# Kernel optimization log

Hardware: AMD Instinct MI355X
Metric: run time of the kernel (lower is better)

Reference implementation:

```python
import jax, jax.numpy as jnp
import numpy as np

N, E, F, B = 4096, 8192, 256, 16


def setup_inputs() -> dict:
    key = jax.random.key(0)
    k_x, k_idx, k_w, k_b = jax.random.split(key, 4)
    x = jax.random.normal(k_x, (B, E, F), dtype=jnp.float32)
    # Incidence matrix: each edge (column) connects 2 random distinct nodes.
    ends = jax.random.randint(k_idx, (2, E), 0, N)  # [2, E] node ids per edge
    cols = jnp.arange(E)
    inci = jnp.zeros((N, E), dtype=jnp.float32)
    inci = inci.at[ends[0], cols].set(1.0).at[ends[1], cols].set(1.0)
    w = jax.random.normal(k_w, (N, E), dtype=jnp.float32) * 0.05
    b = jax.random.normal(k_b, (N, E), dtype=jnp.float32) * 0.01
    return {"x": x, "inci": inci, "w": w, "b": b}


def reference(x, inci, w, b):
    # (w * inci + b) @ x : [N,E] x [B,E,F] -> [B,N,F]
    m = w * inci + b
    return jnp.einsum("ne,bef->bnf", m, x)
```

## Files before the change

kernel.cpp:

```cpp
#include <hip/hip_runtime.h>
#include <hip/hip_bf16.h>

#define Ndim 4096
#define Edim 8192
#define Fdim 256
#define Bdim 16
#define EB (Edim * 2)
#define NT (Edim / 64)

typedef __attribute__((ext_vector_type(8))) short bf16x8;
typedef __attribute__((ext_vector_type(4))) float f32x4;

__device__ __forceinline__ unsigned short f2bf(float f) {
  unsigned int u = __float_as_uint(f);
  u += 0x7fffu + ((u >> 16) & 1u);
  return (unsigned short)(u >> 16);
}

__device__ __forceinline__ void gload_lds16(const void* g, void* l) {
  __builtin_amdgcn_global_load_lds(
      (const __attribute__((address_space(1))) unsigned int*)g,
      (__attribute__((address_space(3))) unsigned int*)l, 16, 0, 0);
}

__device__ __forceinline__ void stage_half(const char* g, char* d) {
  gload_lds16(g, d);
  gload_lds16(g + (size_t)64 * EB, d + 8192);
}

__global__ void convert_m(const float* __restrict__ w, const float* __restrict__ inc,
                          const float* __restrict__ bb, unsigned short* __restrict__ m) {
  size_t i = ((size_t)blockIdx.x * 256 + threadIdx.x) * 4;
  float4 wv = *(const float4*)(w + i);
  float4 iv = *(const float4*)(inc + i);
  float4 bv = *(const float4*)(bb + i);
  ushort4 o;
  o.x = f2bf(fmaf(wv.x, iv.x, bv.x));
  o.y = f2bf(fmaf(wv.y, iv.y, bv.y));
  o.z = f2bf(fmaf(wv.z, iv.z, bv.z));
  o.w = f2bf(fmaf(wv.w, iv.w, bv.w));
  *(ushort4*)(m + i) = o;
}

__global__ void transpose_x(const float* __restrict__ x, unsigned short* __restrict__ xT) {
  __shared__ unsigned short tile[64][66];
  int e0 = blockIdx.x * 64, f0 = blockIdx.y * 64, b = blockIdx.z;
  const float* xb = x + (size_t)b * Edim * Fdim;
  unsigned short* xTb = xT + (size_t)b * Fdim * Edim;
  int t = threadIdx.x;
  int fl = t & 63, rq = t >> 6;
#pragma unroll
  for (int i = 0; i < 16; i++) {
    int el = rq * 16 + i;
    float v = xb[(size_t)(e0 + el) * Fdim + f0 + fl];
    tile[el][fl] = f2bf(v);
  }
  __syncthreads();
  int ep = (t & 31) * 2;
  int fr0 = t >> 5;
#pragma unroll
  for (int j = 0; j < 8; j++) {
    int fr = fr0 + j * 8;
    unsigned int pk = (unsigned int)tile[ep][fr] | ((unsigned int)tile[ep + 1][fr] << 16);
    *(unsigned int*)&xTb[(size_t)(f0 + fr) * Edim + e0 + ep] = pk;
  }
}

template <int STG>
__device__ __forceinline__ void tile_phases(
    const char* lA, const char* lB,
    char* sB, const char* gB,
    char* sA, const char* gA,
    int lane, int wr, int wc, f32x4 acc[8][4]) {
  const int l15 = lane & 15;
  const int khi = (lane >> 4) << 4;
  bf16x8 aLo[8], aHi[8], bLo[4], bHi[4];

#pragma unroll
  for (int m = 0; m < 4; ++m)
#pragma unroll
    for (int kk = 0; kk < 2; ++kk) {
      int r = wr * 128 + m * 16 + l15;
      int cb = kk * 64 + khi;
      aLo[m * 2 + kk] = *(const bf16x8*)(lA + r * 128 + (cb ^ ((r & 7) << 4)));
    }
#pragma unroll
  for (int n = 0; n < 2; ++n)
#pragma unroll
    for (int kk = 0; kk < 2; ++kk) {
      int r = wc * 64 + n * 16 + l15;
      int cb = kk * 64 + khi;
      bLo[n * 2 + kk] = *(const bf16x8*)(lB + r * 128 + (cb ^ ((r & 7) << 4)));
    }
  if constexpr (STG >= 1) stage_half(gB, sB);
  __builtin_amdgcn_s_barrier();
  asm volatile("s_waitcnt lgkmcnt(0)" ::: "memory");
  __builtin_amdgcn_s_setprio(1);
#pragma unroll
  for (int m = 0; m < 4; ++m)
#pragma unroll
    for (int n = 0; n < 2; ++n)
#pragma unroll
      for (int kk = 0; kk < 2; ++kk)
        acc[m][n] = __builtin_amdgcn_mfma_f32_16x16x32_bf16(aLo[m * 2 + kk], bLo[n * 2 + kk],
                                                            acc[m][n], 0, 0, 0);
  __builtin_amdgcn_s_setprio(0);
  __builtin_amdgcn_s_barrier();

#pragma unroll
  for (int n = 0; n < 2; ++n)
#pragma unroll
    for (int kk = 0; kk < 2; ++kk) {
      int r = wc * 64 + (n + 2) * 16 + l15;
      int cb = kk * 64 + khi;
      bHi[n * 2 + kk] = *(const bf16x8*)(lB + r * 128 + (cb ^ ((r & 7) << 4)));
    }
  if constexpr (STG >= 1) stage_half(gB + (size_t)128 * EB, sB + 16384);
  __builtin_amdgcn_s_barrier();
  asm volatile("s_waitcnt lgkmcnt(0)" ::: "memory");
  __builtin_amdgcn_s_setprio(1);
#pragma unroll
  for (int m = 0; m < 4; ++m)
#pragma unroll
    for (int n = 0; n < 2; ++n)
#pragma unroll
      for (int kk = 0; kk < 2; ++kk)
        acc[m][n + 2] = __builtin_amdgcn_mfma_f32_16x16x32_bf16(aLo[m * 2 + kk], bHi[n * 2 + kk],
                                                                acc[m][n + 2], 0, 0, 0);
  __builtin_amdgcn_s_setprio(0);
  __builtin_amdgcn_s_barrier();

#pragma unroll
  for (int m = 0; m < 4; ++m)
#pragma unroll
    for (int kk = 0; kk < 2; ++kk) {
      int r = wr * 128 + 64 + m * 16 + l15;
      int cb = kk * 64 + khi;
      aHi[m * 2 + kk] = *(const bf16x8*)(lA + r * 128 + (cb ^ ((r & 7) << 4)));
    }
  __builtin_amdgcn_s_barrier();
  asm volatile("s_waitcnt lgkmcnt(0)" ::: "memory");
  __builtin_amdgcn_s_setprio(1);
#pragma unroll
  for (int m = 0; m < 4; ++m)
#pragma unroll
    for (int n = 0; n < 2; ++n)
#pragma unroll
      for (int kk = 0; kk < 2; ++kk)
        acc[m + 4][n] = __builtin_amdgcn_mfma_f32_16x16x32_bf16(aHi[m * 2 + kk], bLo[n * 2 + kk],
                                                                acc[m + 4][n], 0, 0, 0);
  __builtin_amdgcn_s_setprio(0);
  __builtin_amdgcn_s_barrier();

  if constexpr (STG == 2) {
    stage_half(gA, sA);
    stage_half(gA + (size_t)128 * EB, sA + 16384);
  }
  __builtin_amdgcn_s_barrier();
  __builtin_amdgcn_s_setprio(1);
#pragma unroll
  for (int m = 0; m < 4; ++m)
#pragma unroll
    for (int n = 0; n < 2; ++n)
#pragma unroll
      for (int kk = 0; kk < 2; ++kk)
        acc[m + 4][n + 2] = __builtin_amdgcn_mfma_f32_16x16x32_bf16(aHi[m * 2 + kk], bHi[n * 2 + kk],
                                                                    acc[m + 4][n + 2], 0, 0, 0);
  __builtin_amdgcn_s_setprio(0);
  if constexpr (STG == 2) asm volatile("s_waitcnt vmcnt(4)" ::: "memory");
  if constexpr (STG == 1) asm volatile("s_waitcnt vmcnt(0)" ::: "memory");
  __builtin_amdgcn_s_barrier();
}

__global__ __launch_bounds__(512, 2) void gemm8(
    const unsigned short* __restrict__ A,
    const unsigned short* __restrict__ Bt,
    float* __restrict__ C) {
  __shared__ __align__(16) char smem[131072];

  const int bid = blockIdx.x;
  const int lid = ((bid & 7) << 5) | (bid >> 3);
  const int mt = lid >> 4;
  const int bb = lid & 15;

  const int tid = threadIdx.x;
  const int lane = tid & 63;
  const int w = tid >> 6;
  const int wr = w >> 2;
  const int wc = w & 3;

  const int r0 = tid >> 3;
  const int c0 = ((tid & 7) ^ (r0 & 7)) << 4;

  const char* Ag = (const char*)A + (size_t)(mt * 256) * EB + (size_t)r0 * EB + c0;
  const char* Bg = (const char*)Bt + (size_t)(bb * 256) * EB + (size_t)r0 * EB + c0;
  char* dst = smem + tid * 16;

  f32x4 acc[8][4];
#pragma unroll
  for (int m = 0; m < 8; ++m)
#pragma unroll
    for (int n = 0; n < 4; ++n) acc[m][n] = (f32x4){0.f, 0.f, 0.f, 0.f};

  stage_half(Ag, dst);
  stage_half(Ag + (size_t)128 * EB, dst + 16384);
  stage_half(Bg, dst + 32768);
  stage_half(Bg + (size_t)128 * EB, dst + 49152);
  stage_half(Ag + 128, dst + 65536);
  stage_half(Ag + 128 + (size_t)128 * EB, dst + 81920);
  asm volatile("s_waitcnt vmcnt(4)" ::: "memory");
  __builtin_amdgcn_s_barrier();

  for (int t = 0; t < NT - 2; ++t) {
    const int u = t & 1;
    const char* lA = smem + u * 65536;
    const char* lB = lA + 32768;
    char* sB = dst + (u ^ 1) * 65536 + 32768;
    char* sA = dst + u * 65536;
    const char* gB = Bg + (size_t)(t + 1) * 128;
    const char* gA = Ag + (size_t)(t + 2) * 128;
    tile_phases<2>(lA, lB, sB, gB, sA, gA, lane, wr, wc, acc);
  }
  {
    const int u = (NT - 2) & 1;
    tile_phases<1>(smem + u * 65536, smem + u * 65536 + 32768,
                   dst + (u ^ 1) * 65536 + 32768, Bg + (size_t)(NT - 1) * 128,
                   nullptr, nullptr, lane, wr, wc, acc);
    tile_phases<0>(smem + (u ^ 1) * 65536, smem + (u ^ 1) * 65536 + 32768,
                   nullptr, nullptr, nullptr, nullptr, lane, wr, wc, acc);
  }

  float* Cb = C + (size_t)bb * (Ndim * Fdim) + (size_t)(mt * 256) * Fdim;
#pragma unroll
  for (int m = 0; m < 8; ++m) {
    int row0 = wr * 128 + m * 16 + ((lane >> 4) << 2);
#pragma unroll
    for (int n = 0; n < 4; ++n) {
      int col = wc * 64 + n * 16 + (lane & 15);
#pragma unroll
      for (int j = 0; j < 4; ++j)
        Cb[(size_t)(row0 + j) * Fdim + col] = acc[m][n][j];
    }
  }
}

__global__ void naive_kernel(const float* __restrict__ x, const float* __restrict__ inci,
                             const float* __restrict__ w, const float* __restrict__ b,
                             float* __restrict__ out) {
  int n = blockIdx.x & (Ndim - 1);
  int bb = blockIdx.x >> 12;
  int f = threadIdx.x;
  const float* xb = x + (size_t)bb * Edim * Fdim;
  const size_t nE = (size_t)n * Edim;
  float acc = 0.f;
  for (int e = 0; e < Edim; e++) {
    float m = fmaf(w[nE + e], inci[nE + e], b[nE + e]);
    acc = fmaf(m, xb[(size_t)e * Fdim + f], acc);
  }
  out[(size_t)bb * Ndim * Fdim + (size_t)n * Fdim + f] = acc;
}

extern "C" void kernel_launch(void* const* d_in, const int* in_sizes, int n_in,
                              void* d_out, int out_size, void* d_ws, size_t ws_size,
                              hipStream_t stream) {
  const float* x = (const float*)d_in[0];
  const float* inci = (const float*)d_in[1];
  const float* w = (const float*)d_in[2];
  const float* b = (const float*)d_in[3];
  float* out = (float*)d_out;

  size_t mBytes = (size_t)Ndim * Edim * 2;
  size_t xTBytes = (size_t)Bdim * Fdim * Edim * 2;
  if (ws_size >= mBytes + xTBytes) {
    unsigned short* m_bf = (unsigned short*)d_ws;
    unsigned short* xT = m_bf + (size_t)Ndim * Edim;
    convert_m<<<(Ndim * (size_t)Edim) / 4 / 256, 256, 0, stream>>>(w, inci, b, m_bf);
    transpose_x<<<dim3(Edim / 64, Fdim / 64, Bdim), 256, 0, stream>>>(x, xT);
    gemm8<<<256, 512, 0, stream>>>(m_bf, xT, out);
  } else {
    naive_kernel<<<Bdim * Ndim, 256, 0, stream>>>(x, inci, w, b, out);
  }
}
```

Baseline: 345.7 us.

## Restructure GEMM prefetch schedule to stream A and B tiles across four phases

Reworks the double-buffered K-loop so each k-tile issues four half-tile global-to-LDS loads, one in each MFMA phase. The next A tile and the B tile two steps ahead now go into the freed buffer halves, instead of B one step ahead and a doubled A load in the last phase. The loop is unrolled by two so buffer offsets are compile-time constants. A partial lgkmcnt wait is added before the first barrier. The aim is to spread global load issue evenly across the phases and cut stalls, at the cost of more delicate buffer-reuse ordering.

```diff
diff --git a/kernel.cpp b/kernel.cpp
--- a/kernel.cpp
+++ b/kernel.cpp
@@ -27,6 +27,9 @@
   gload_lds16(g, d);
   gload_lds16(g + (size_t)64 * EB, d + 8192);
 }
+
+#define RD(base, r, kk) \
+  (*(const bf16x8*)((base) + (r) * 128 + ((((kk) * 64) + khi) ^ (((r) & 7) << 4))))
 
 __global__ void convert_m(const float* __restrict__ w, const float* __restrict__ inc,
                           const float* __restrict__ bb, unsigned short* __restrict__ m) {
@@ -66,11 +69,11 @@
   }
 }
 
-template <int STG>
-__device__ __forceinline__ void tile_phases(
+template <bool S1, bool S2, bool S3, bool S4, int VM>
+__device__ __forceinline__ void ktile(
     const char* lA, const char* lB,
-    char* sB, const char* gB,
-    char* sA, const char* gA,
+    char* d1, const char* g1, char* d2, const char* g2,
+    char* d3, const char* g3, char* d4, const char* g4,
     int lane, int wr, int wc, f32x4 acc[8][4]) {
   const int l15 = lane & 15;
   const int khi = (lane >> 4) << 4;
@@ -79,20 +82,15 @@
 #pragma unroll
   for (int m = 0; m < 4; ++m)
 #pragma unroll
-    for (int kk = 0; kk < 2; ++kk) {
-      int r = wr * 128 + m * 16 + l15;
-      int cb = kk * 64 + khi;
-      aLo[m * 2 + kk] = *(const bf16x8*)(lA + r * 128 + (cb ^ ((r & 7) << 4)));
-    }
+    for (int kk = 0; kk < 2; ++kk)
+      aLo[m * 2 + kk] = RD(lA, wr * 128 + m * 16 + l15, kk);
 #pragma unroll
   for (int n = 0; n < 2; ++n)
 #pragma unroll
-    for (int kk = 0; kk < 2; ++kk) {
-      int r = wc * 64 + n * 16 + l15;
-      int cb = kk * 64 + khi;
-      bLo[n * 2 + kk] = *(const bf16x8*)(lB + r * 128 + (cb ^ ((r & 7) << 4)));
-    }
-  if constexpr (STG >= 1) stage_half(gB, sB);
+    for (int kk = 0; kk < 2; ++kk)
+      bLo[n * 2 + kk] = RD(lB, wc * 64 + n * 16 + l15, kk);
+  if constexpr (S1) stage_half(g1, d1);
+  asm volatile("s_waitcnt lgkmcnt(8)" ::: "memory");
   __builtin_amdgcn_s_barrier();
   asm volatile("s_waitcnt lgkmcnt(0)" ::: "memory");
   __builtin_amdgcn_s_setprio(1);
@@ -110,12 +108,9 @@
 #pragma unroll
   for (int n = 0; n < 2; ++n)
 #pragma unroll
-    for (int kk = 0; kk < 2; ++kk) {
-      int r = wc * 64 + (n + 2) * 16 + l15;
-      int cb = kk * 64 + khi;
-      bHi[n * 2 + kk] = *(const bf16x8*)(lB + r * 128 + (cb ^ ((r & 7) << 4)));
-    }
-  if constexpr (STG >= 1) stage_half(gB + (size_t)128 * EB, sB + 16384);
+    for (int kk = 0; kk < 2; ++kk)
+      bHi[n * 2 + kk] = RD(lB, wc * 64 + (n + 2) * 16 + l15, kk);
+  if constexpr (S2) stage_half(g2, d2);
   __builtin_amdgcn_s_barrier();
   asm volatile("s_waitcnt lgkmcnt(0)" ::: "memory");
   __builtin_amdgcn_s_setprio(1);
@@ -133,11 +128,9 @@
 #pragma unroll
   for (int m = 0; m < 4; ++m)
 #pragma unroll
-    for (int kk = 0; kk < 2; ++kk) {
-      int r = wr * 128 + 64 + m * 16 + l15;
-      int cb = kk * 64 + khi;
-      aHi[m * 2 + kk] = *(const bf16x8*)(lA + r * 128 + (cb ^ ((r & 7) << 4)));
-    }
+    for (int kk = 0; kk < 2; ++kk)
+      aHi[m * 2 + kk] = RD(lA, wr * 128 + 64 + m * 16 + l15, kk);
+  if constexpr (S3) stage_half(g3, d3);
   __builtin_amdgcn_s_barrier();
   asm volatile("s_waitcnt lgkmcnt(0)" ::: "memory");
   __builtin_amdgcn_s_setprio(1);
@@ -152,10 +145,7 @@
   __builtin_amdgcn_s_setprio(0);
   __builtin_amdgcn_s_barrier();
 
-  if constexpr (STG == 2) {
-    stage_half(gA, sA);
-    stage_half(gA + (size_t)128 * EB, sA + 16384);
-  }
+  if constexpr (S4) stage_half(g4, d4);
   __builtin_amdgcn_s_barrier();
   __builtin_amdgcn_s_setprio(1);
 #pragma unroll
@@ -167,8 +157,8 @@
         acc[m + 4][n + 2] = __builtin_amdgcn_mfma_f32_16x16x32_bf16(aHi[m * 2 + kk], bHi[n * 2 + kk],
                                                                     acc[m + 4][n + 2], 0, 0, 0);
   __builtin_amdgcn_s_setprio(0);
-  if constexpr (STG == 2) asm volatile("s_waitcnt vmcnt(4)" ::: "memory");
-  if constexpr (STG == 1) asm volatile("s_waitcnt vmcnt(0)" ::: "memory");
+  if constexpr (VM == 4) asm volatile("s_waitcnt vmcnt(4)" ::: "memory");
+  if constexpr (VM == 0) asm volatile("s_waitcnt vmcnt(0)" ::: "memory");
   __builtin_amdgcn_s_barrier();
 }
 
@@ -202,32 +192,45 @@
 #pragma unroll
     for (int n = 0; n < 4; ++n) acc[m][n] = (f32x4){0.f, 0.f, 0.f, 0.f};
 
+  const size_t HEB = (size_t)128 * EB;
+
   stage_half(Ag, dst);
-  stage_half(Ag + (size_t)128 * EB, dst + 16384);
+  stage_half(Ag + HEB, dst + 16384);
   stage_half(Bg, dst + 32768);
-  stage_half(Bg + (size_t)128 * EB, dst + 49152);
-  stage_half(Ag + 128, dst + 65536);
-  stage_half(Ag + 128 + (size_t)128 * EB, dst + 81920);
+  stage_half(Bg + HEB, dst + 49152);
+  stage_half(Bg + 128, dst + 98304);
+  stage_half(Bg + 128 + HEB, dst + 114688);
   asm volatile("s_waitcnt vmcnt(4)" ::: "memory");
   __builtin_amdgcn_s_barrier();
 
-  for (int t = 0; t < NT - 2; ++t) {
-    const int u = t & 1;
-    const char* lA = smem + u * 65536;
-    const char* lB = lA + 32768;
-    char* sB = dst + (u ^ 1) * 65536 + 32768;
-    char* sA = dst + u * 65536;
-    const char* gB = Bg + (size_t)(t + 1) * 128;
-    const char* gA = Ag + (size_t)(t + 2) * 128;
-    tile_phases<2>(lA, lB, sB, gB, sA, gA, lane, wr, wc, acc);
+  for (int i = 0; i < NT / 2 - 1; ++i) {
+    const size_t t1b = (size_t)(2 * i + 1) * 128;
+    const size_t t2b = (size_t)(2 * i + 2) * 128;
+    const size_t t3b = (size_t)(2 * i + 3) * 128;
+    ktile<1, 1, 1, 1, 4>(smem, smem + 32768,
+                         dst + 65536, Ag + t1b,
+                         dst + 81920, Ag + t1b + HEB,
+                         dst + 32768, Bg + t2b,
+                         dst + 49152, Bg + t2b + HEB,
+                         lane, wr, wc, acc);
+    ktile<1, 1, 1, 1, 4>(smem + 65536, smem + 98304,
+                         dst, Ag + t2b,
+                         dst + 16384, Ag + t2b + HEB,
+                         dst + 98304, Bg + t3b,
+                         dst + 114688, Bg + t3b + HEB,
+                         lane, wr, wc, acc);
   }
   {
-    const int u = (NT - 2) & 1;
-    tile_phases<1>(smem + u * 65536, smem + u * 65536 + 32768,
-                   dst + (u ^ 1) * 65536 + 32768, Bg + (size_t)(NT - 1) * 128,
-                   nullptr, nullptr, lane, wr, wc, acc);
-    tile_phases<0>(smem + (u ^ 1) * 65536, smem + (u ^ 1) * 65536 + 32768,
-                   nullptr, nullptr, nullptr, nullptr, lane, wr, wc, acc);
+    const size_t tlb = (size_t)(NT - 1) * 128;
+    ktile<1, 1, 0, 0, 0>(smem, smem + 32768,
+                         dst + 65536, Ag + tlb,
+                         dst + 81920, Ag + tlb + HEB,
+                         nullptr, nullptr, nullptr, nullptr,
+                         lane, wr, wc, acc);
+    ktile<0, 0, 0, 0, -1>(smem + 65536, smem + 98304,
+                          nullptr, nullptr, nullptr, nullptr,
+                          nullptr, nullptr, nullptr, nullptr,
+                          lane, wr, wc, acc);
   }
 
   float* Cb = C + (size_t)bb * (Ndim * Fdim) + (size_t)(mt * 256) * Fdim;
```

Result: faster. 334.4 us (-3.3%).
